# Kernel optimization log

Hardware: AMD Instinct MI355X
Metric: run time of the kernel (lower is better)

## Reference

```python
import jax, jax.numpy as jnp
import numpy as np

B, D, H, O, E = 8192, 1024, 4096, 1024, 3

def setup_inputs() -> dict:
    key = jax.random.key(0)
    ks = jax.random.split(key, 8)
    s = lambda fan_in: 1.0 / np.sqrt(fan_in)
    return {
        "x":   jax.random.normal(ks[0], (B, D), jnp.float32),
        "gw1": jax.random.normal(ks[1], (D, 256), jnp.float32) * s(D),
        "gb1": jnp.zeros((256,), jnp.float32),
        "gw2": jax.random.normal(ks[2], (256, 128), jnp.float32) * s(256),
        "gb2": jnp.zeros((128,), jnp.float32),
        "gw3": jax.random.normal(ks[3], (128, E), jnp.float32) * s(128),
        "gb3": jnp.zeros((E,), jnp.float32),
        "ew1": jax.random.normal(ks[4], (E, D, H), jnp.float32) * s(D),
        "eb1": jnp.zeros((E, H), jnp.float32),
        "ew2": jax.random.normal(ks[5], (E, H, O), jnp.float32) * s(H),
        "eb2": jnp.zeros((E, O), jnp.float32),
        "top_k": 2,
    }

def reference(x, gw1, gb1, gw2, gb2, gw3, gb3, ew1, eb1, ew2, eb2, top_k):
    # Gating network (dropout is identity in eval mode)
    g = jax.nn.relu(x @ gw1 + gb1)
    g = jax.nn.relu(g @ gw2 + gb2)
    gates = jax.nn.softmax(g @ gw3 + gb3, axis=-1)          # [B, E]

    # top-k routing with renormalized weights
    topk_scores, topk_idx = jax.lax.top_k(gates, top_k)     # [B, k]
    topk_scores = topk_scores / jnp.sum(topk_scores, axis=-1, keepdims=True)

    # scatter normalized scores into dense [B, E] combine weights
    b_ix = jnp.arange(x.shape[0])[:, None]
    combine = jnp.zeros_like(gates).at[b_ix, topk_idx].add(topk_scores)  # [B, E]

    # run all experts densely (small E=3), combine with routing weights
    eh = jax.nn.relu(jnp.einsum('bd,edh->beh', x, ew1) + eb1[None])      # [B, E, H]
    eo = jnp.einsum('beh,eho->beo', eh, ew2) + eb2[None]                 # [B, E, O]
    out = jnp.einsum('be,beo->bo', combine, eo)                          # [B, O]
    return out, gates
```

## Files before the change

kernel.cpp:

```cpp
#include <hip/hip_runtime.h>
#include <cstdint>
#include <cstddef>

#define B_ROWS 8192
#define D_DIM  1024
#define H_DIM  4096
#define O_DIM  1024
#define E_NUM  3
#define K2     (2 * H_DIM)
#define MT256  34
#define SLOT_MAX (MT256 * 256)
#define OSPLIT 8

typedef __attribute__((ext_vector_type(4))) float f4;
typedef __attribute__((ext_vector_type(8))) _Float16 half8;

__device__ __forceinline__ unsigned short f2h_bits(float f) {
  _Float16 h = (_Float16)f;
  return __builtin_bit_cast(unsigned short, h);
}

__device__ __forceinline__ void async16(const void* g, void* l) {
  __builtin_amdgcn_global_load_lds(
      (const __attribute__((address_space(1))) unsigned int*)g,
      (__attribute__((address_space(3))) unsigned int*)l, 16, 0, 0);
}

__global__ __launch_bounds__(256) void k_cast_x(const float* __restrict__ in,
                                                unsigned short* __restrict__ out) {
  size_t i = (size_t)blockIdx.x * 256 + threadIdx.x;
  const f4* p = (const f4*)in;
  f4 a = p[2 * i], b = p[2 * i + 1];
  half8 h;
#pragma unroll
  for (int j = 0; j < 4; ++j) { h[j] = (_Float16)a[j]; h[4 + j] = (_Float16)b[j]; }
  *(half8*)(out + 8 * i) = h;
}

__global__ __launch_bounds__(256) void k_transpose_cast(const float* __restrict__ in,
                                                        unsigned short* __restrict__ out,
                                                        int R, int C) {
  __shared__ float tile[32][33];
  const size_t eoff = (size_t)blockIdx.z * R * C;
  const float* I = in + eoff;
  unsigned short* O = out + eoff;
  int c0 = blockIdx.x * 32, r0 = blockIdx.y * 32;
  int tx = threadIdx.x & 31, ty = threadIdx.x >> 5;
#pragma unroll
  for (int i = 0; i < 4; ++i)
    tile[ty + 8 * i][tx] = I[(size_t)(r0 + ty + 8 * i) * C + c0 + tx];
  __syncthreads();
#pragma unroll
  for (int i = 0; i < 4; ++i)
    O[(size_t)(c0 + ty + 8 * i) * R + r0 + tx] = f2h_bits(tile[tx][ty + 8 * i]);
}

__global__ __launch_bounds__(256) void k_gemm_f32(const float* __restrict__ A,
                                                  const float* __restrict__ Bm,
                                                  const float* __restrict__ bias,
                                                  float* __restrict__ C,
                                                  int N, int K) {
  __shared__ float sAT[16][68];
  __shared__ float sB[16][68];
  const int t = threadIdx.x;
  const int tx = t & 15, ty = t >> 4;
  const int m0 = blockIdx.y * 64, n0 = blockIdx.x * 64;
  float acc[4][4] = {};
  for (int k0 = 0; k0 < K; k0 += 16) {
    __syncthreads();
#pragma unroll
    for (int i = 0; i < 4; ++i) {
      int idx = t + i * 256;
      int r = idx >> 4, c = idx & 15;
      sAT[c][r] = A[(size_t)(m0 + r) * K + (k0 + c)];
      int rb = idx >> 6, cb = idx & 63;
      sB[rb][cb] = Bm[(size_t)(k0 + rb) * N + (n0 + cb)];
    }
    __syncthreads();
#pragma unroll
    for (int kk = 0; kk < 16; ++kk) {
      f4 av = *(const f4*)&sAT[kk][ty * 4];
      f4 bv = *(const f4*)&sB[kk][tx * 4];
#pragma unroll
      for (int i = 0; i < 4; ++i)
#pragma unroll
        for (int j = 0; j < 4; ++j)
          acc[i][j] = fmaf(av[i], bv[j], acc[i][j]);
    }
  }
#pragma unroll
  for (int i = 0; i < 4; ++i) {
    int row = m0 + ty * 4 + i;
    f4 v;
#pragma unroll
    for (int j = 0; j < 4; ++j)
      v[j] = fmaxf(acc[i][j] + bias[n0 + tx * 4 + j], 0.f);
    *(f4*)&C[(size_t)row * N + n0 + tx * 4] = v;
  }
}

__global__ __launch_bounds__(256) void k_gate_topk(const float* __restrict__ h2,
                                                   const float* __restrict__ gw3,
                                                   const float* __restrict__ gb3,
                                                   float* __restrict__ gates,
                                                   float* __restrict__ combine,
                                                   int* __restrict__ bucket) {
  const int lane = threadIdx.x & 63;
  const int row = blockIdx.x * 4 + (threadIdx.x >> 6);
  const float* h = h2 + (size_t)row * 128;
  float h0 = h[lane], h1 = h[lane + 64];
  float l0 = h0 * gw3[lane * 3 + 0] + h1 * gw3[(lane + 64) * 3 + 0];
  float l1 = h0 * gw3[lane * 3 + 1] + h1 * gw3[(lane + 64) * 3 + 1];
  float l2 = h0 * gw3[lane * 3 + 2] + h1 * gw3[(lane + 64) * 3 + 2];
#pragma unroll
  for (int off = 32; off > 0; off >>= 1) {
    l0 += __shfl_down(l0, off);
    l1 += __shfl_down(l1, off);
    l2 += __shfl_down(l2, off);
  }
  if (lane == 0) {
    float g0 = l0 + gb3[0], g1v = l1 + gb3[1], g2v = l2 + gb3[2];
    float mx = fmaxf(g0, fmaxf(g1v, g2v));
    float e0 = expf(g0 - mx), e1 = expf(g1v - mx), e2 = expf(g2v - mx);
    float inv = 1.f / (e0 + e1 + e2);
    float p0 = e0 * inv, p1 = e1 * inv, p2 = e2 * inv;
    gates[row * 3 + 0] = p0; gates[row * 3 + 1] = p1; gates[row * 3 + 2] = p2;
    int amin = 0; float pm = p0;
    if (p1 <= pm) { pm = p1; amin = 1; }
    if (p2 <= pm) { pm = p2; amin = 2; }
    float denom = (p0 + p1 + p2) - pm;
    combine[row * 3 + 0] = (amin == 0) ? 0.f : p0 / denom;
    combine[row * 3 + 1] = (amin == 1) ? 0.f : p1 / denom;
    combine[row * 3 + 2] = (amin == 2) ? 0.f : p2 / denom;
    bucket[row] = amin;
  }
}

__global__ __launch_bounds__(256) void k_count(const int* __restrict__ bucket,
                                               int* __restrict__ cnt) {
  int row = blockIdx.x * 256 + threadIdx.x;
  int b = bucket[row];
  int lane = threadIdx.x & 63;
#pragma unroll
  for (int bid = 0; bid < 3; ++bid) {
    unsigned long long m = __ballot(b == bid);
    if (m && b == bid) {
      int prefix = __popcll(m & ((1ull << lane) - 1));
      if (prefix == 0) atomicAdd(&cnt[bid], __popcll(m));
    }
  }
}

__global__ void k_meta(const int* __restrict__ cnt, int* __restrict__ meta,
                       int* __restrict__ cnt2) {
  int t0 = (cnt[0] + 255) >> 8;
  int t1 = (cnt[1] + 255) >> 8;
  int t2 = (cnt[2] + 255) >> 8;
  meta[0] = 0; meta[1] = t0; meta[2] = t0 + t1; meta[3] = t0 + t1 + t2;
  cnt2[0] = 0; cnt2[1] = 0; cnt2[2] = 0;
}

__global__ __launch_bounds__(256) void k_scatter(const int* __restrict__ bucket,
                                                 const int* __restrict__ meta,
                                                 int* __restrict__ cnt2,
                                                 int* __restrict__ sorted) {
  int row = blockIdx.x * 256 + threadIdx.x;
  int b = bucket[row];
  int lane = threadIdx.x & 63;
#pragma unroll
  for (int bid = 0; bid < 3; ++bid) {
    unsigned long long m = __ballot(b == bid);
    if (m) {
      int cntm = __popcll(m);
      int leader = __ffsll((unsigned long long)m) - 1;
      int base = 0;
      if (lane == leader) base = atomicAdd(&cnt2[bid], cntm);
      base = __shfl(base, leader);
      if (b == bid) {
        int prefix = __popcll(m & ((1ull << lane) - 1));
        sorted[meta[bid] * 256 + base + prefix] = row;
      }
    }
  }
}

__device__ __forceinline__ void bucket_experts(int b, int& ea, int& eb) {
  ea = (b == 0) ? 1 : 0;
  eb = (b == 2) ? 1 : 2;
}


#define BAR8()  do { __builtin_amdgcn_s_barrier(); __builtin_amdgcn_sched_barrier(0); } while (0)
#define LGKM0() do { asm volatile("s_waitcnt lgkmcnt(0)" ::: "memory"); __builtin_amdgcn_sched_barrier(0); } while (0)
#define VMW(n)  do { asm volatile("s_waitcnt vmcnt(" #n ")" ::: "memory"); __builtin_amdgcn_sched_barrier(0); } while (0)

#define STG_A(buf, h, kt) do { \
    async16(aptr[(h) * 2 + 0] + (size_t)(kt) * 64, smem + (buf) * 32768 + (h) * 16384 + t * 16); \
    async16(aptr[(h) * 2 + 1] + (size_t)(kt) * 64, smem + (buf) * 32768 + (h) * 16384 + 8192 + t * 16); \
  } while (0)
#define STG_B(buf, h, kt) do { \
    async16(bptr[(h) * 2 + 0] + (size_t)(kt) * 64, smem + 65536 + (buf) * 32768 + (h) * 16384 + t * 16); \
    async16(bptr[(h) * 2 + 1] + (size_t)(kt) * 64, smem + 65536 + (buf) * 32768 + (h) * 16384 + 8192 + t * 16); \
  } while (0)
#define LDA8(buf, mh) do { \
    _Pragma("unroll") \
    for (int mf = 0; mf < 4; ++mf) { \
      fa[mf][0] = *(const half8*)(smem + (buf) * 32768 + baseA + (mh) * 8192 + mf * 2048 + ck0); \
      fa[mf][1] = *(const half8*)(smem + (buf) * 32768 + baseA + (mh) * 8192 + mf * 2048 + ck1); \
    } } while (0)
#define LDB8(buf, nh) do { \
    _Pragma("unroll") \
    for (int nf2 = 0; nf2 < 2; ++nf2) { \
      fb[(nh) * 2 + nf2][0] = *(const half8*)(smem + (buf) * 32768 + baseB + ((nh) * 2 + nf2) * 2048 + ck0); \
      fb[(nh) * 2 + nf2][1] = *(const half8*)(smem + (buf) * 32768 + baseB + ((nh) * 2 + nf2) * 2048 + ck1); \
    } } while (0)
#define MM8(mh, nh) do { \
    _Pragma("unroll") \
    for (int mf = 0; mf < 4; ++mf) { \
      _Pragma("unroll") \
      for (int nf2 = 0; nf2 < 2; ++nf2) { \
        acc[(mh) * 4 + mf][(nh) * 2 + nf2] = __builtin_amdgcn_mfma_f32_16x16x32_f16( \
            fa[mf][0], fb[(nh) * 2 + nf2][0], acc[(mh) * 4 + mf][(nh) * 2 + nf2], 0, 0, 0); \
        acc[(mh) * 4 + mf][(nh) * 2 + nf2] = __builtin_amdgcn_mfma_f32_16x16x32_f16( \
            fa[mf][1], fb[(nh) * 2 + nf2][1], acc[(mh) * 4 + mf][(nh) * 2 + nf2], 0, 0, 0); \
      } } } while (0)

#define KLOOP8(NITER, LASTKT) \
  _Pragma("unroll 1") \
  for (int it = 0; it < (NITER) - 1; ++it) { \
    const int kt = 2 * it; \
    LDA8(0, 0); LDB8(0, 0); STG_A(1, 0, kt + 1); \
    BAR8(); LGKM0(); \
    __builtin_amdgcn_s_setprio(1); MM8(0, 0); __builtin_amdgcn_s_setprio(0); \
    BAR8(); \
    LDB8(0, 1); STG_A(1, 1, kt + 1); \
    BAR8(); LGKM0(); \
    __builtin_amdgcn_s_setprio(1); MM8(0, 1); __builtin_amdgcn_s_setprio(0); \
    BAR8(); \
    LDA8(0, 1); STG_B(0, 0, kt + 2); \
    BAR8(); LGKM0(); \
    __builtin_amdgcn_s_setprio(1); MM8(1, 0); __builtin_amdgcn_s_setprio(0); \
    BAR8(); \
    STG_A(0, 0, kt + 2); \
    BAR8(); LGKM0(); \
    __builtin_amdgcn_s_setprio(1); MM8(1, 1); __builtin_amdgcn_s_setprio(0); \
    VMW(4); BAR8(); \
    LDA8(1, 0); LDB8(1, 0); STG_A(0, 1, kt + 2); \
    BAR8(); LGKM0(); \
    __builtin_amdgcn_s_setprio(1); MM8(0, 0); __builtin_amdgcn_s_setprio(0); \
    BAR8(); \
    LDB8(1, 1); STG_B(0, 1, kt + 2); \
    BAR8(); LGKM0(); \
    __builtin_amdgcn_s_setprio(1); MM8(0, 1); __builtin_amdgcn_s_setprio(0); \
    BAR8(); \
    LDA8(1, 1); STG_B(1, 0, kt + 3); \
    BAR8(); LGKM0(); \
    __builtin_amdgcn_s_setprio(1); MM8(1, 0); __builtin_amdgcn_s_setprio(0); \
    BAR8(); \
    STG_B(1, 1, kt + 3); \
    BAR8(); LGKM0(); \
    __builtin_amdgcn_s_setprio(1); MM8(1, 1); __builtin_amdgcn_s_setprio(0); \
    VMW(4); BAR8(); \
  } \
  {  \
    LDA8(0, 0); LDB8(0, 0); STG_A(1, 0, LASTKT); \
    BAR8(); LGKM0(); \
    __builtin_amdgcn_s_setprio(1); MM8(0, 0); __builtin_amdgcn_s_setprio(0); \
    BAR8(); \
    LDB8(0, 1); STG_A(1, 1, LASTKT); \
    BAR8(); LGKM0(); \
    __builtin_amdgcn_s_setprio(1); MM8(0, 1); __builtin_amdgcn_s_setprio(0); \
    BAR8(); \
    LDA8(0, 1); \
    BAR8(); LGKM0(); \
    __builtin_amdgcn_s_setprio(1); MM8(1, 0); __builtin_amdgcn_s_setprio(0); \
    BAR8(); \
    BAR8(); LGKM0(); \
    __builtin_amdgcn_s_setprio(1); MM8(1, 1); __builtin_amdgcn_s_setprio(0); \
    VMW(0); BAR8(); \
    LDA8(1, 0); LDB8(1, 0); MM8(0, 0); \
    LDB8(1, 1); MM8(0, 1); \
    LDA8(1, 1); MM8(1, 0); \
    MM8(1, 1); \
  }

__global__ __launch_bounds__(512, 2) void k_expert_h8(const unsigned short* __restrict__ Xh,
                                                      const unsigned short* __restrict__ W1T,
                                                      const float* __restrict__ combine,
                                                      const float* __restrict__ eb1,
                                                      const int* __restrict__ sorted,
                                                      const int* __restrict__ meta,
                                                      unsigned short* __restrict__ EHS) {
  constexpr int K = D_DIM;
  const int mt = blockIdx.x;
  const int tb1 = meta[1], tb2 = meta[2], tb3 = meta[3];
  if (mt >= tb3) return;
  const int b = (mt >= tb2) ? 2 : (mt >= tb1) ? 1 : 0;
  int ea, ebx; bucket_experts(b, ea, ebx);
  const int z = blockIdx.z;
  const int e = z ? ebx : ea;
  const int slot0 = mt * 256;
  const int n0 = blockIdx.y * 256;

  __shared__ __align__(16) char smem[131072];
  __shared__ float sC[256];
  const int t = threadIdx.x;
  if (t < 256) {
    int r = sorted[slot0 + t];
    sC[t] = (r < 0) ? 0.f : combine[(size_t)r * 3 + e];
  }

  const int jrow = t >> 3;
  const int j = (t & 7) ^ (jrow & 7);
  const unsigned short* aptr[4];
  const unsigned short* bptr[4];
#pragma unroll
  for (int i = 0; i < 4; ++i) {
    int R = jrow + i * 64;
    int r = sorted[slot0 + R];
    int rr = (r < 0) ? 0 : r;
    aptr[i] = Xh + (size_t)rr * K + j * 8;
    bptr[i] = W1T + (size_t)e * H_DIM * K + (size_t)(n0 + R) * K + j * 8;
  }
  const int lane = t & 63;
  const int wid = t >> 6;
  const int wm = wid >> 2, wn = wid & 3;
  const int quad = lane >> 4, l16 = lane & 15;
  const int ck0 = ((quad) ^ (l16 & 7)) * 16;
  const int ck1 = ((4 + quad) ^ (l16 & 7)) * 16;
  const int baseA = (wm * 128 + l16) * 128;
  const int baseB = 65536 + (wn * 64 + l16) * 128;

  f4 acc[8][4] = {};
  half8 fa[4][2], fb[4][2];

  STG_A(0, 0, 0); STG_A(0, 1, 0); STG_B(0, 0, 0); STG_B(0, 1, 0);
  STG_B(1, 0, 1); STG_B(1, 1, 1);
  VMW(4); BAR8();

  KLOOP8(8, 15)

  const float* bias = eb1 + (size_t)e * H_DIM;
#pragma unroll
  for (int nf = 0; nf < 4; ++nf) {
    int col = n0 + wn * 64 + nf * 16 + l16;
    float bb = bias[col];
#pragma unroll
    for (int mf = 0; mf < 8; ++mf) {
#pragma unroll
      for (int r = 0; r < 4; ++r) {
        int rloc = wm * 128 + mf * 16 + quad * 4 + r;
        float v = fmaxf(acc[mf][nf][r] + bb, 0.f) * sC[rloc];
        EHS[(size_t)(slot0 + rloc) * K2 + (size_t)z * H_DIM + col] = f2h_bits(v);
      }
    }
  }
}

__global__ __launch_bounds__(512, 2) void k_expert_o8(const unsigned short* __restrict__ EHS,
                                                      const unsigned short* __restrict__ W2T,
                                                      const float* __restrict__ combine,
                                                      const float* __restrict__ eb2,
                                                      const int* __restrict__ sorted,
                                                      const int* __restrict__ meta,
                                                      float* __restrict__ OUT) {
  const int mt = blockIdx.x;
  const int tb1 = meta[1], tb2 = meta[2], tb3 = meta[3];
  if (mt >= tb3) return;
  const int b = (mt >= tb2) ? 2 : (mt >= tb1) ? 1 : 0;
  int ea, ebx; bucket_experts(b, ea, ebx);
  const int hz = blockIdx.z;
  const int e = (hz < 4) ? ea : ebx;
  const int slot0 = mt * 256;
  const int n0 = blockIdx.y * 256;

  __shared__ __align__(16) char smem[131072];
  __shared__ int sRow[256];
  __shared__ float sCa[256], sCb[256];
  const int t = threadIdx.x;
  if (t < 256) {
    int r = sorted[slot0 + t];
    sRow[t] = r;
    int rr = (r < 0) ? 0 : r;
    sCa[t] = combine[(size_t)rr * 3 + ea];
    sCb[t] = combine[(size_t)rr * 3 + ebx];
  }

  const int jrow = t >> 3;
  const int j = (t & 7) ^ (jrow & 7);
  const unsigned short* aptr[4];
  const unsigned short* bptr[4];
#pragma unroll
  for (int i = 0; i < 4; ++i) {
    int R = jrow + i * 64;
    aptr[i] = EHS + (size_t)(slot0 + R) * K2 + (size_t)hz * 1024 + j * 8;
    bptr[i] = W2T + (size_t)e * O_DIM * H_DIM + (size_t)(n0 + R) * H_DIM + (size_t)(hz & 3) * 1024 + j * 8;
  }
  const int lane = t & 63;
  const int wid = t >> 6;
  const int wm = wid >> 2, wn = wid & 3;
  const int quad = lane >> 4, l16 = lane & 15;
  const int ck0 = ((quad) ^ (l16 & 7)) * 16;
  const int ck1 = ((4 + quad) ^ (l16 & 7)) * 16;
  const int baseA = (wm * 128 + l16) * 128;
  const int baseB = 65536 + (wn * 64 + l16) * 128;

  f4 acc[8][4] = {};
  half8 fa[4][2], fb[4][2];

  STG_A(0, 0, 0); STG_A(0, 1, 0); STG_B(0, 0, 0); STG_B(0, 1, 0);
  STG_B(1, 0, 1); STG_B(1, 1, 1);
  VMW(4); BAR8();

  KLOOP8(8, 15)

#pragma unroll
  for (int nf = 0; nf < 4; ++nf) {
    int col = n0 + wn * 64 + nf * 16 + l16;
    float ba = eb2[(size_t)ea * O_DIM + col];
    float bb = eb2[(size_t)ebx * O_DIM + col];
#pragma unroll
    for (int mf = 0; mf < 8; ++mf) {
#pragma unroll
      for (int r = 0; r < 4; ++r) {
        int rloc = wm * 128 + mf * 16 + quad * 4 + r;
        int rowg = sRow[rloc];
        if (rowg >= 0) {
          float v = acc[mf][nf][r];
          if (hz == 0) v += sCa[rloc] * ba + sCb[rloc] * bb;
          atomicAdd(&OUT[(size_t)rowg * O_DIM + col], v);
        }
      }
    }
  }
}

extern "C" void kernel_launch(void* const* d_in, const int* in_sizes, int n_in,
                              void* d_out, int out_size, void* d_ws, size_t ws_size,
                              hipStream_t stream) {
  const float* x   = (const float*)d_in[0];
  const float* gw1 = (const float*)d_in[1];
  const float* gb1 = (const float*)d_in[2];
  const float* gw2 = (const float*)d_in[3];
  const float* gb2 = (const float*)d_in[4];
  const float* gw3 = (const float*)d_in[5];
  const float* gb3 = (const float*)d_in[6];
  const float* ew1 = (const float*)d_in[7];
  const float* eb1 = (const float*)d_in[8];
  const float* ew2 = (const float*)d_in[9];
  const float* eb2 = (const float*)d_in[10];
  float* out = (float*)d_out;
  float* gates = out + (size_t)B_ROWS * O_DIM;

  char* ws = (char*)d_ws;
  size_t off = 0;
  auto take = [&](size_t bytes) -> char* {
    char* p = ws + off;
    off += (bytes + 255) & ~(size_t)255;
    return p;
  };
  unsigned short* xh  = (unsigned short*)take((size_t)B_ROWS * D_DIM * 2);
  unsigned short* w1t = (unsigned short*)take((size_t)E_NUM * H_DIM * D_DIM * 2);
  unsigned short* w2t = (unsigned short*)take((size_t)E_NUM * O_DIM * H_DIM * 2);
  float* comb   = (float*)take((size_t)B_ROWS * 3 * 4);
  float* g1     = (float*)take((size_t)B_ROWS * 256 * 4);
  float* h2     = (float*)take((size_t)B_ROWS * 128 * 4);
  int* bucket   = (int*)take((size_t)B_ROWS * 4);
  int* sorted   = (int*)take((size_t)SLOT_MAX * 4);
  int* cnt      = (int*)take(3 * 4);
  int* cnt2     = (int*)take(3 * 4);
  int* meta     = (int*)take(4 * 4);
  unsigned short* ehs = (unsigned short*)take((size_t)SLOT_MAX * K2 * 2);

  hipMemsetAsync(cnt, 0, 3 * 4, stream);
  hipMemsetAsync(sorted, 0xFF, (size_t)SLOT_MAX * 4, stream);
  hipMemsetAsync(out, 0, (size_t)B_ROWS * O_DIM * 4, stream);

  k_cast_x<<<dim3(B_ROWS * D_DIM / (256 * 8)), 256, 0, stream>>>(x, xh);
  k_transpose_cast<<<dim3(H_DIM / 32, D_DIM / 32, E_NUM), 256, 0, stream>>>(ew1, w1t, D_DIM, H_DIM);
  k_transpose_cast<<<dim3(O_DIM / 32, H_DIM / 32, E_NUM), 256, 0, stream>>>(ew2, w2t, H_DIM, O_DIM);

  k_gemm_f32<<<dim3(256 / 64, B_ROWS / 64), 256, 0, stream>>>(x, gw1, gb1, g1, 256, D_DIM);
  k_gemm_f32<<<dim3(128 / 64, B_ROWS / 64), 256, 0, stream>>>(g1, gw2, gb2, h2, 128, 256);
  k_gate_topk<<<dim3(B_ROWS / 4), 256, 0, stream>>>(h2, gw3, gb3, gates, comb, bucket);

  k_count<<<dim3(B_ROWS / 256), 256, 0, stream>>>(bucket, cnt);
  k_meta<<<1, 1, 0, stream>>>(cnt, meta, cnt2);
  k_scatter<<<dim3(B_ROWS / 256), 256, 0, stream>>>(bucket, meta, cnt2, sorted);

  k_expert_h8<<<dim3(MT256, H_DIM / 256, 2), 512, 0, stream>>>(
      xh, w1t, comb, eb1, sorted, meta, ehs);
  k_expert_o8<<<dim3(MT256, O_DIM / 256, OSPLIT), 512, 0, stream>>>(
      ehs, w2t, comb, eb2, sorted, meta, out);
}
```

Before: 811.6 us.

## Replace split-K atomics with per-split partial buffers and a reduction kernel

The second expert GEMM now splits K into 4 parts instead of 8 and has a runtime osplit parameter. Each split stores its result into its own partial output buffer in workspace, and a new vectorized kernel sums the partials. This removes the float atomicAdd traffic on the output and the memset of the output. In exchange it adds partial-buffer writes and a reduction pass, and the smaller grid may fill the device less evenly. If workspace is too small, it falls back to two splits with atomics.

```diff
diff --git a/kernel.cpp b/kernel.cpp
--- a/kernel.cpp
+++ b/kernel.cpp
@@ -10,7 +10,6 @@
 #define K2     (2 * H_DIM)
 #define MT256  34
 #define SLOT_MAX (MT256 * 256)
-#define OSPLIT 8
 
 typedef __attribute__((ext_vector_type(4))) float f4;
 typedef __attribute__((ext_vector_type(8))) _Float16 half8;
@@ -363,14 +362,18 @@
                                                       const float* __restrict__ eb2,
                                                       const int* __restrict__ sorted,
                                                       const int* __restrict__ meta,
-                                                      float* __restrict__ OUT) {
+                                                      float* __restrict__ dst,
+                                                      int osplit, int use_atomic) {
   const int mt = blockIdx.x;
   const int tb1 = meta[1], tb2 = meta[2], tb3 = meta[3];
   if (mt >= tb3) return;
   const int b = (mt >= tb2) ? 2 : (mt >= tb1) ? 1 : 0;
   int ea, ebx; bucket_experts(b, ea, ebx);
   const int hz = blockIdx.z;
-  const int e = (hz < 4) ? ea : ebx;
+  const int half = osplit >> 1;
+  const int e = (hz < half) ? ea : ebx;
+  const int kchunk = K2 / osplit;
+  const int koff_b = (hz % half) * kchunk;
   const int slot0 = mt * 256;
   const int n0 = blockIdx.y * 256;
 
@@ -393,8 +396,8 @@
 #pragma unroll
   for (int i = 0; i < 4; ++i) {
     int R = jrow + i * 64;
-    aptr[i] = EHS + (size_t)(slot0 + R) * K2 + (size_t)hz * 1024 + j * 8;
-    bptr[i] = W2T + (size_t)e * O_DIM * H_DIM + (size_t)(n0 + R) * H_DIM + (size_t)(hz & 3) * 1024 + j * 8;
+    aptr[i] = EHS + (size_t)(slot0 + R) * K2 + (size_t)hz * kchunk + j * 8;
+    bptr[i] = W2T + (size_t)e * O_DIM * H_DIM + (size_t)(n0 + R) * H_DIM + koff_b + j * 8;
   }
   const int lane = t & 63;
   const int wid = t >> 6;
@@ -412,8 +415,11 @@
   STG_B(1, 0, 1); STG_B(1, 1, 1);
   VMW(4); BAR8();
 
-  KLOOP8(8, 15)
-
+  const int niter = kchunk / 128;
+  const int lastkt = 2 * niter - 1;
+  KLOOP8(niter, lastkt)
+
+  float* part = use_atomic ? dst : dst + (size_t)hz * B_ROWS * O_DIM;
 #pragma unroll
   for (int nf = 0; nf < 4; ++nf) {
     int col = n0 + wn * 64 + nf * 16 + l16;
@@ -428,11 +434,22 @@
         if (rowg >= 0) {
           float v = acc[mf][nf][r];
           if (hz == 0) v += sCa[rloc] * ba + sCb[rloc] * bb;
-          atomicAdd(&OUT[(size_t)rowg * O_DIM + col], v);
+          if (use_atomic) atomicAdd(&part[(size_t)rowg * O_DIM + col], v);
+          else            part[(size_t)rowg * O_DIM + col] = v;
         }
       }
     }
   }
+}
+
+__global__ __launch_bounds__(256) void k_reduceN(const float* __restrict__ parts,
+                                                 float* __restrict__ out, int n) {
+  const size_t S = (size_t)B_ROWS * O_DIM;
+  size_t i = ((size_t)blockIdx.x * 256 + threadIdx.x) * 4;
+  f4 v = *(const f4*)(parts + i);
+#pragma unroll 1
+  for (int p = 1; p < n; ++p) v += *(const f4*)(parts + (size_t)p * S + i);
+  *(f4*)(out + i) = v;
 }
 
 extern "C" void kernel_launch(void* const* d_in, const int* in_sizes, int n_in,
@@ -472,9 +489,24 @@
   int* meta     = (int*)take(4 * 4);
   unsigned short* ehs = (unsigned short*)take((size_t)SLOT_MAX * K2 * 2);
 
+  const size_t part_bytes = (size_t)B_ROWS * O_DIM * 4;
+  int osplit, use_atomic;
+  float* o8_dst;
+  if (off + 4 * part_bytes + 1024 <= ws_size) {
+    osplit = 4; use_atomic = 0;
+    o8_dst = (float*)take(4 * part_bytes);
+  } else if (off + 2 * part_bytes + 1024 <= ws_size) {
+    osplit = 2; use_atomic = 0;
+    o8_dst = (float*)take(2 * part_bytes);
+  } else {
+    osplit = 2; use_atomic = 1;
+    o8_dst = out;
+  }
+
   hipMemsetAsync(cnt, 0, 3 * 4, stream);
   hipMemsetAsync(sorted, 0xFF, (size_t)SLOT_MAX * 4, stream);
-  hipMemsetAsync(out, 0, (size_t)B_ROWS * O_DIM * 4, stream);
+  if (use_atomic)
+    hipMemsetAsync(out, 0, (size_t)B_ROWS * O_DIM * 4, stream);
 
   k_cast_x<<<dim3(B_ROWS * D_DIM / (256 * 8)), 256, 0, stream>>>(x, xh);
   k_transpose_cast<<<dim3(H_DIM / 32, D_DIM / 32, E_NUM), 256, 0, stream>>>(ew1, w1t, D_DIM, H_DIM);
@@ -490,6 +522,8 @@
 
   k_expert_h8<<<dim3(MT256, H_DIM / 256, 2), 512, 0, stream>>>(
       xh, w1t, comb, eb1, sorted, meta, ehs);
-  k_expert_o8<<<dim3(MT256, O_DIM / 256, OSPLIT), 512, 0, stream>>>(
-      ehs, w2t, comb, eb2, sorted, meta, out);
-}
+  k_expert_o8<<<dim3(MT256, O_DIM / 256, osplit), 512, 0, stream>>>(
+      ehs, w2t, comb, eb2, sorted, meta, o8_dst, osplit, use_atomic);
+  if (!use_atomic)
+    k_reduceN<<<dim3(B_ROWS * O_DIM / (256 * 4)), 256, 0, stream>>>(o8_dst, out, osplit);
+}
```

Measured after the change: 751.5 us. 1.08x faster.
